# Optimization experiments

Hardware: AMD Instinct MI355X
Metric: run time of the kernel (lower is better)

## Reference

```python
import jax, jax.numpy as jnp
import numpy as np

B, T, D = 2, 2048, 1024
H, HKV, HD = 16, 4, 64
N_REP = H // HKV
SKIP_WINDOW, GLOBAL_TOKENS = 24, 8
NEG_INF = -1.0e9
ROPE_BASE = 10000.0


def rope_tables(seq_len, head_dim):
    # timm build_rotary_pos_embed (in_pixels=False, 1 spatial dim): dim//4 freq bands,
    # repeat_interleave(2) -> head_dim//2, then cat twice -> head_dim.
    nb = head_dim // 4
    inv_freq = 1.0 / (ROPE_BASE ** (jnp.arange(nb, dtype=jnp.float32) / nb))
    ang = jnp.arange(seq_len, dtype=jnp.float32)[:, None] * inv_freq[None, :]  # [T, nb]
    sin_h = jnp.repeat(jnp.sin(ang), 2, axis=-1)  # [T, HD/2]
    cos_h = jnp.repeat(jnp.cos(ang), 2, axis=-1)
    sin = jnp.concatenate([sin_h, sin_h], axis=-1)  # [T, HD]
    cos = jnp.concatenate([cos_h, cos_h], axis=-1)
    return cos, sin


def rotate_half(x):
    x1, x2 = jnp.split(x, 2, axis=-1)
    return jnp.concatenate([-x2, x1], axis=-1)


def apply_rope(x, cos, sin):
    # x: [B, H, T, HD]; cos/sin: [T, HD]
    return x * cos[None, None] + rotate_half(x) * sin[None, None]


def skip_mask(seq_len):
    half_window = SKIP_WINDOW // 2
    i = jnp.arange(seq_len)[:, None]
    j = jnp.arange(seq_len)[None, :]
    allowed = (jnp.abs(i - j) <= half_window) | (i < GLOBAL_TOKENS) | (j < GLOBAL_TOKENS)
    return jnp.where(allowed, 0.0, NEG_INF).astype(jnp.float32)  # [T, T]


def setup_inputs() -> dict:
    key = jax.random.key(0)
    ks = jax.random.split(key, 10)
    s = 0.02
    return {
        "x": jax.random.normal(ks[0], (B, T, D), jnp.float32),
        "Wq": jax.random.normal(ks[1], (D, D), jnp.float32) * s,
        "bq": jax.random.normal(ks[2], (D,), jnp.float32) * s,
        "Wk": jax.random.normal(ks[3], (D, HKV * HD), jnp.float32) * s,
        "bk": jax.random.normal(ks[4], (HKV * HD,), jnp.float32) * s,
        "Wv": jax.random.normal(ks[5], (D, HKV * HD), jnp.float32) * s,
        "bv": jax.random.normal(ks[6], (HKV * HD,), jnp.float32) * s,
        "Wo": jax.random.normal(ks[7], (D, D), jnp.float32) * s,
        "bo": jax.random.normal(ks[8], (D,), jnp.float32) * s,
        "head_weights": 1.0 + jax.random.normal(ks[9], (H,), jnp.float32) * 0.1,
    }


def reference(x, Wq, bq, Wk, bk, Wv, bv, Wo, bo, head_weights):
    Bx, Tx, _ = x.shape
    q = (x @ Wq + bq).reshape(Bx, Tx, H, HD).transpose(0, 2, 1, 3)       # [B,H,T,HD]
    k = (x @ Wk + bk).reshape(Bx, Tx, HKV, HD).transpose(0, 2, 1, 3)     # [B,HKV,T,HD]
    v = (x @ Wv + bv).reshape(Bx, Tx, HKV, HD).transpose(0, 2, 1, 3)

    cos, sin = rope_tables(Tx, HD)
    q = apply_rope(q, cos, sin)
    k = apply_rope(k, cos, sin)

    # GQA: repeat kv heads (each kv head gets n_rep consecutive q-head copies)
    k = jnp.repeat(k, N_REP, axis=1)  # [B,H,T,HD]
    v = jnp.repeat(v, N_REP, axis=1)

    # per-head learned q scaling
    q = q * head_weights[None, :, None, None]

    mask = skip_mask(Tx)  # [T,T], additive
    scale = 1.0 / jnp.sqrt(jnp.float32(HD))
    scores = jnp.einsum("bhqd,bhkd->bhqk", q, k) * scale + mask[None, None]
    attn = jax.nn.softmax(scores, axis=-1)
    out = jnp.einsum("bhqk,bhkd->bhqd", attn, v)          # [B,H,T,HD]
    out = out.transpose(0, 2, 1, 3).reshape(Bx, Tx, D)    # [B,T,D]
    return out @ Wo + bo
```

## Files before the change

### kernel.cpp

```cpp
#include <hip/hip_runtime.h>
#include <hip/hip_bf16.h>
#include <math.h>

typedef short bf16x8 __attribute__((ext_vector_type(8)));
typedef float f32x4 __attribute__((ext_vector_type(4)));
typedef unsigned short u16;
typedef u16 u16x4 __attribute__((ext_vector_type(4)));
typedef u16 u16x8 __attribute__((ext_vector_type(8)));

#define DEV static __device__ __forceinline__
#define GLB __attribute__((address_space(1)))
#define LDS __attribute__((address_space(3)))

#if defined(__has_builtin)
#if __has_builtin(__builtin_amdgcn_fdot2_f32_bf16)
#define HAS_BF16_DOT2 1
#endif
#endif

#ifdef HAS_BF16_DOT2
typedef __bf16 bf16x2 __attribute__((ext_vector_type(2)));
#endif

DEV float bf2f(u16 u) { union { unsigned int i; float f; } v; v.i = ((unsigned int)u) << 16; return v.f; }
DEV u16 f2bf(float f) {
  union { float fl; unsigned int i; } v; v.fl = f;
  return (u16)((v.i + 0x7FFFu + ((v.i >> 16) & 1u)) >> 16);
}

DEV float dot8(u16x8 k, u16x8 q, float acc) {
#ifdef HAS_BF16_DOT2
  union { u16x8 u; bf16x2 b[4]; } ku, qu;
  ku.u = k; qu.u = q;
#pragma unroll
  for (int e = 0; e < 4; ++e)
    acc = __builtin_amdgcn_fdot2_f32_bf16(ku.b[e], qu.b[e], acc, false);
#else
#pragma unroll
  for (int e = 0; e < 8; ++e) acc = fmaf(bf2f(k[e]), bf2f(q[e]), acc);
#endif
  return acc;
}

__global__ __launch_bounds__(256) void prepw_kernel(
    const float* __restrict__ x, const float* __restrict__ bq,
    const float* __restrict__ bk, const float* __restrict__ bv,
    float* __restrict__ biascat, float* __restrict__ cosT, float* __restrict__ sinT,
    u16* __restrict__ xbf,
    const float* __restrict__ wq, const float* __restrict__ wk,
    const float* __restrict__ wv, const float* __restrict__ wo,
    u16* __restrict__ wcat, u16* __restrict__ wot)
{
  __shared__ float tile[32][33];
  if (blockIdx.x < 4358) {
    int idx = blockIdx.x * 256 + threadIdx.x;
    const int NX = (4096 * 1024) / 4;
    if (idx < NX) {
      const float4 v = ((const float4*)x)[idx];
      u16x4 o;
      o[0] = f2bf(v.x); o[1] = f2bf(v.y); o[2] = f2bf(v.z); o[3] = f2bf(v.w);
      *((u16x4*)xbf + idx) = o;
    } else if (idx < NX + 1536) {
      int n = idx - NX;
      biascat[n] = (n < 1024) ? bq[n] : (n < 1280 ? bk[n - 1024] : bv[n - 1280]);
    } else if (idx < NX + 1536 + 65536) {
      int e = idx - NX - 1536;
      int t = e >> 5, dh = e & 31;
      double invf = pow(10000.0, -(double)(dh >> 1) / 16.0);
      double ang = (double)t * invf;
      cosT[e] = (float)cos(ang);
      sinT[e] = (float)sin(ang);
    }
  } else {
    const int idx = blockIdx.x - 4358;
    const int z = idx >> 10;
    const int rem = idx & 1023;
    const int bx = rem & 31, by = rem >> 5;
    const float* src; u16* dst; int N; int roff;
    if (z == 0)      { src = wq; dst = wcat; N = 1024; roff = 0; }
    else if (z == 1) { src = wk; dst = wcat; N = 256;  roff = 1024; }
    else if (z == 2) { src = wv; dst = wcat; N = 256;  roff = 1280; }
    else             { src = wo; dst = wot;  N = 1024; roff = 0; }
    const int n0 = bx << 5;
    if (n0 >= N) return;
    const int k0 = by << 5;
    const int tx = threadIdx.x & 31, ty = threadIdx.x >> 5;
#pragma unroll
    for (int r = 0; r < 32; r += 8)
      tile[ty + r][tx] = src[(size_t)(k0 + ty + r) * N + n0 + tx];
    __syncthreads();
#pragma unroll
    for (int r = 0; r < 32; r += 8)
      dst[((size_t)(roff + n0 + ty + r) << 10) + k0 + tx] = f2bf(tile[tx][ty + r]);
  }
}

__global__ __launch_bounds__(256) void gemm_kernel(
    const u16* __restrict__ A, const u16* __restrict__ Bt, int K, int mode,
    const float* __restrict__ bias_cat, u16* __restrict__ qbuf, u16* __restrict__ kbufT,
    u16* __restrict__ vbufT, const float* __restrict__ bo, float* __restrict__ outp,
    const float* __restrict__ cosT, const float* __restrict__ sinT,
    const float* __restrict__ hw)
{
  __shared__ alignas(16) char ldsA[16384];
  __shared__ alignas(16) char ldsB[8192];
  const int tid = threadIdx.x;
  const int lane = tid & 63, wid = tid >> 6;
  const int l15 = lane & 15, lg = lane >> 4;
  const int wm = wid << 5;
  const size_t K_ = (size_t)K;
  const u16* Apan = A + (size_t)blockIdx.y * 128 * K_;
  const u16* Bpan = Bt + (size_t)blockIdx.x * 64 * K_;

  f32x4 acc[2][4];
  const f32x4 fz = {0.f, 0.f, 0.f, 0.f};
#pragma unroll
  for (int mt = 0; mt < 2; ++mt)
#pragma unroll
    for (int nt = 0; nt < 4; ++nt) acc[mt][nt] = fz;

  for (int k0 = 0; k0 < K; k0 += 64) {
#pragma unroll
    for (int i = 0; i < 4; ++i) {
      const int grp = i * 4 + wid;
      const int c = grp * 64 + lane;
      const int r = c >> 3, k8 = (c & 7) << 3;
      const u16* ga = Apan + (size_t)r * K_ + k0 + k8;
      __builtin_amdgcn_global_load_lds((const GLB void*)ga, (LDS void*)(ldsA + grp * 1024), 16, 0, 0);
      if (i < 2) {
        const u16* gb = Bpan + (size_t)r * K_ + k0 + k8;
        __builtin_amdgcn_global_load_lds((const GLB void*)gb, (LDS void*)(ldsB + grp * 1024), 16, 0, 0);
      }
    }
    __syncthreads();
#pragma unroll
    for (int ks = 0; ks < 2; ++ks) {
      const int kbyte = ks * 64 + lg * 16;
      bf16x8 af[2], bfr[4];
#pragma unroll
      for (int mt = 0; mt < 2; ++mt)
        af[mt] = *(const bf16x8*)(ldsA + (wm + mt * 16 + l15) * 128 + kbyte);
#pragma unroll
      for (int nt = 0; nt < 4; ++nt)
        bfr[nt] = *(const bf16x8*)(ldsB + (nt * 16 + l15) * 128 + kbyte);
#pragma unroll
      for (int mt = 0; mt < 2; ++mt)
#pragma unroll
        for (int nt = 0; nt < 4; ++nt)
          acc[mt][nt] = __builtin_amdgcn_mfma_f32_16x16x32_bf16(af[mt], bfr[nt], acc[mt][nt], 0, 0, 0);
    }
    __syncthreads();
  }

  const int rb = blockIdx.y * 128 + wm + (lg << 2);
  const int bx = blockIdx.x;

  if (mode == 0) {
    const bool isQ = (bx < 16);
    const bool isV = (bx >= 20);
    const float hws = isQ ? hw[bx] * 0.125f : 1.0f;
    float bia[4];
#pragma unroll
    for (int nt = 0; nt < 4; ++nt) bia[nt] = bias_cat[bx * 64 + l15 + nt * 16];
    if (isV) {
#pragma unroll
      for (int mt = 0; mt < 2; ++mt) {
        const int r0 = rb + mt * 16;
        const int bb = r0 >> 11, t0 = r0 & 2047;
        const size_t base = ((size_t)(bb * 4 + (bx - 20))) << 17;
#pragma unroll
        for (int nt = 0; nt < 4; ++nt) {
          u16x4 pk;
#pragma unroll
          for (int j = 0; j < 4; ++j) pk[j] = f2bf(acc[mt][nt][j] + bia[nt]);
          const int d = l15 + nt * 16;
          *(u16x4*)(vbufT + base + (size_t)d * 2048 + t0) = pk;
        }
      }
    } else {
#pragma unroll
      for (int mt = 0; mt < 2; ++mt) {
#pragma unroll
        for (int j = 0; j < 4; ++j) {
          const int r = rb + mt * 16 + j;
          const int bb = r >> 11, t = r & 2047;
          float z[4];
#pragma unroll
          for (int nt = 0; nt < 4; ++nt) z[nt] = acc[mt][nt][j] + bia[nt];
          const float c0 = cosT[(t << 5) + l15],      s0 = sinT[(t << 5) + l15];
          const float c1 = cosT[(t << 5) + l15 + 16], s1 = sinT[(t << 5) + l15 + 16];
          const float n0 = (z[0] * c0 - z[2] * s0) * hws;
          const float n2 = (z[2] * c0 + z[0] * s0) * hws;
          const float n1 = (z[1] * c1 - z[3] * s1) * hws;
          const float n3 = (z[3] * c1 + z[1] * s1) * hws;
          z[0] = n0; z[1] = n1; z[2] = n2; z[3] = n3;
#pragma unroll
          for (int nt = 0; nt < 4; ++nt) {
            const int d = l15 + nt * 16;
            const u16 val = f2bf(z[nt]);
            if (isQ) {
              qbuf[(((size_t)(bb * 16 + bx) * 2048 + t) << 6) + d] = val;
            } else {
              kbufT[(((size_t)(bb * 4 + (bx - 16))) << 17) + ((d >> 3) << 14) + (t << 3) + (d & 7)] = val;
            }
          }
        }
      }
    }
  } else {
#pragma unroll
    for (int nt = 0; nt < 4; ++nt) {
      const int c = bx * 64 + l15 + nt * 16;
      const float bias = bo[c];
#pragma unroll
      for (int mt = 0; mt < 2; ++mt) {
#pragma unroll
        for (int j = 0; j < 4; ++j) {
          const int r = rb + mt * 16 + j;
          outp[(size_t)r * 1024 + c] = acc[mt][nt][j] + bias;
        }
      }
    }
  }
}

__global__ __launch_bounds__(256) void attn_band_kernel(
    const u16* __restrict__ qbuf, const u16* __restrict__ kbufT,
    const u16* __restrict__ vbufT, u16* __restrict__ obuf)
{
  __shared__ alignas(16) u16 plds[4][16][64];
  const int tid = threadIdx.x;
  const int lane = tid & 63, w = tid >> 6;
  const int l15 = lane & 15, lg = lane >> 4;
  const f32x4 fz = {0.f, 0.f, 0.f, 0.f};
  u16* pw = (u16*)plds[w];

  const int gw = blockIdx.x * 4 + w;
  const int k = gw & 127;
  const int h = (gw >> 7) & 15;
  const int b = gw >> 11;
  const int i0 = 8 + k * 16;
  const int a = i0 - 16;
  const int hkv = h >> 2;

  const u16* KpT = kbufT + (((size_t)(b * 4 + hkv)) << 17);
  const u16* VpT = vbufT + (((size_t)(b * 4 + hkv)) << 17);
  const u16* Qp  = qbuf + (((size_t)(b * 16 + h)) << 17);

  bf16x8 qa[2];
#pragma unroll
  for (int ch = 0; ch < 2; ++ch)
    qa[ch] = *(const bf16x8*)(Qp + (size_t)(i0 + l15) * 64 + ch * 32 + lg * 8);

  int slotj[4];
#pragma unroll
  for (int mt = 0; mt < 4; ++mt) {
    const int t = mt * 16 + l15;
    int j = (t < 8) ? t : a + t - 8;
    slotj[mt] = j < 0 ? 0 : (j > 2047 ? 2047 : j);
  }

  f32x4 s[4];
#pragma unroll
  for (int mt = 0; mt < 4; ++mt) s[mt] = fz;
#pragma unroll
  for (int ch = 0; ch < 2; ++ch) {
#pragma unroll
    for (int mt = 0; mt < 4; ++mt) {
      bf16x8 kf = *(const bf16x8*)(KpT + ((size_t)(ch * 4 + lg) << 14) + (slotj[mt] << 3));
      s[mt] = __builtin_amdgcn_mfma_f32_16x16x32_bf16(qa[ch], kf, s[mt], 0, 0, 0);
    }
  }

#pragma unroll
  for (int mt = 0; mt < 4; ++mt) {
    const int t = mt * 16 + l15;
    const int j = (t < 8) ? t : a + t - 8;
#pragma unroll
    for (int jr = 0; jr < 4; ++jr) {
      const int i = i0 + lg * 4 + jr;
      bool ok;
      if (t < 8) ok = true;
      else ok = (j >= 8) && (j < 2048) && (j >= i - 12) && (j <= i + 12);
      if (!ok) s[mt][jr] = -1e30f;
    }
  }
  float pinvl[4];
#pragma unroll
  for (int jr = 0; jr < 4; ++jr) {
    float m = fmaxf(fmaxf(s[0][jr], s[1][jr]), fmaxf(s[2][jr], s[3][jr]));
#pragma unroll
    for (int sh = 1; sh <= 8; sh <<= 1) m = fmaxf(m, __shfl_xor(m, sh));
    float sum = 0.f;
#pragma unroll
    for (int mt = 0; mt < 4; ++mt) {
      const float p = __expf(s[mt][jr] - m);
      s[mt][jr] = p;
      sum += p;
    }
#pragma unroll
    for (int sh = 1; sh <= 8; sh <<= 1) sum += __shfl_xor(sum, sh);
    pinvl[jr] = 1.f / sum;
  }

#pragma unroll
  for (int mt = 0; mt < 4; ++mt) {
    const int t = mt * 16 + l15;
#pragma unroll
    for (int jr = 0; jr < 4; ++jr) {
      const int q = lg * 4 + jr;
      pw[q * 64 + (t ^ ((q & 7) << 3))] = f2bf(s[mt][jr] * pinvl[jr]);
    }
  }

  bf16x8 paf[2];
#pragma unroll
  for (int ch = 0; ch < 2; ++ch)
    paf[ch] = *(const bf16x8*)(pw + l15 * 64 + ((ch * 32 + lg * 8) ^ ((l15 & 7) << 3)));

  f32x4 oacc[4];
#pragma unroll
  for (int db = 0; db < 4; ++db) oacc[db] = fz;
  __builtin_amdgcn_s_setprio(1);
#pragma unroll
  for (int db = 0; db < 4; ++db) {
#pragma unroll
    for (int ch = 0; ch < 2; ++ch) {
      const int sl0 = ch * 32 + lg * 8;
      int j0 = (sl0 < 8) ? 0 : a + sl0 - 8;
      j0 = j0 < 0 ? 0 : (j0 > 2040 ? 2040 : j0);
      bf16x8 vf = *(const bf16x8*)(VpT + (size_t)(db * 16 + l15) * 2048 + j0);
      oacc[db] = __builtin_amdgcn_mfma_f32_16x16x32_bf16(paf[ch], vf, oacc[db], 0, 0, 0);
    }
  }
  __builtin_amdgcn_s_setprio(0);

#pragma unroll
  for (int jr = 0; jr < 4; ++jr) {
    const int i = i0 + lg * 4 + jr;
    if (i < 2048) {
      const size_t rowo = ((size_t)(b * 2048 + i)) << 10;
#pragma unroll
      for (int db = 0; db < 4; ++db)
        obuf[rowo + h * 64 + db * 16 + l15] = f2bf(oacc[db][jr]);
    }
  }
}

__global__ __launch_bounds__(64) void attn_globp_kernel(
    const u16* __restrict__ qbuf, const u16* __restrict__ kbufT,
    const u16* __restrict__ vbufT,
    float* __restrict__ pm, float* __restrict__ pl, float* __restrict__ po)
{
  __shared__ alignas(16) u16 plds[16][64];
  const int kc = blockIdx.x;
  const int hkv = blockIdx.y & 3;
  const int i = blockIdx.y >> 2;
  const int b = blockIdx.z;
  const int lane = threadIdx.x;
  const u16* KpT = kbufT + (((size_t)(b * 4 + hkv)) << 17);
  const u16* VpT = vbufT + (((size_t)(b * 4 + hkv)) << 17);
  const u16* Qr0 = qbuf + ((((size_t)(b * 16 + hkv * 4 + 0)) * 2048 + i) << 6);
  const u16* Qr1 = qbuf + ((((size_t)(b * 16 + hkv * 4 + 1)) * 2048 + i) << 6);
  const u16* Qr2 = qbuf + ((((size_t)(b * 16 + hkv * 4 + 2)) * 2048 + i) << 6);
  const u16* Qr3 = qbuf + ((((size_t)(b * 16 + hkv * 4 + 3)) * 2048 + i) << 6);

  const int j = (kc << 6) + lane;
  float s0 = 0.f, s1 = 0.f, s2 = 0.f, s3 = 0.f;
#pragma unroll
  for (int d8 = 0; d8 < 8; ++d8) {
    u16x8 k8 = *(const u16x8*)(KpT + (d8 << 14) + (j << 3));
    u16x8 q0 = *(const u16x8*)(Qr0 + d8 * 8);
    u16x8 q1 = *(const u16x8*)(Qr1 + d8 * 8);
    u16x8 q2 = *(const u16x8*)(Qr2 + d8 * 8);
    u16x8 q3 = *(const u16x8*)(Qr3 + d8 * 8);
    s0 = dot8(k8, q0, s0);
    s1 = dot8(k8, q1, s1);
    s2 = dot8(k8, q2, s2);
    s3 = dot8(k8, q3, s3);
  }
  float m0 = s0, m1 = s1, m2 = s2, m3 = s3;
#pragma unroll
  for (int sh = 32; sh >= 1; sh >>= 1) {
    m0 = fmaxf(m0, __shfl_xor(m0, sh));
    m1 = fmaxf(m1, __shfl_xor(m1, sh));
    m2 = fmaxf(m2, __shfl_xor(m2, sh));
    m3 = fmaxf(m3, __shfl_xor(m3, sh));
  }
  float p0 = __expf(s0 - m0), p1 = __expf(s1 - m1), p2 = __expf(s2 - m2), p3 = __expf(s3 - m3);
  float l0 = p0, l1 = p1, l2 = p2, l3 = p3;
#pragma unroll
  for (int sh = 32; sh >= 1; sh >>= 1) {
    l0 += __shfl_xor(l0, sh);
    l1 += __shfl_xor(l1, sh);
    l2 += __shfl_xor(l2, sh);
    l3 += __shfl_xor(l3, sh);
  }

  u16* pw = (u16*)plds;
  pw[0 * 64 + (lane ^ 0)]  = f2bf(p0);
  pw[1 * 64 + (lane ^ 8)]  = f2bf(p1);
  pw[2 * 64 + (lane ^ 16)] = f2bf(p2);
  pw[3 * 64 + (lane ^ 24)] = f2bf(p3);

  const int l15 = lane & 15, lg = lane >> 4;
  bf16x8 paf[2];
#pragma unroll
  for (int ch = 0; ch < 2; ++ch)
    paf[ch] = *(const bf16x8*)(pw + l15 * 64 + ((ch * 32 + lg * 8) ^ ((l15 & 7) << 3)));

  f32x4 oacc[4];
  const f32x4 fz = {0.f, 0.f, 0.f, 0.f};
#pragma unroll
  for (int db = 0; db < 4; ++db) oacc[db] = fz;
#pragma unroll
  for (int db = 0; db < 4; ++db) {
#pragma unroll
    for (int ch = 0; ch < 2; ++ch) {
      const int j0 = (kc << 6) + ch * 32 + lg * 8;
      bf16x8 vf = *(const bf16x8*)(VpT + (size_t)(db * 16 + l15) * 2048 + j0);
      oacc[db] = __builtin_amdgcn_mfma_f32_16x16x32_bf16(paf[ch], vf, oacc[db], 0, 0, 0);
    }
  }

  const int part = (((b * 4 + hkv) * 8 + i) << 5) + kc;
  if (lane == 0) {
    pm[part * 4 + 0] = m0; pm[part * 4 + 1] = m1; pm[part * 4 + 2] = m2; pm[part * 4 + 3] = m3;
    pl[part * 4 + 0] = l0; pl[part * 4 + 1] = l1; pl[part * 4 + 2] = l2; pl[part * 4 + 3] = l3;
  }
  if (lg == 0) {
    float* pob = po + (((size_t)part << 2) << 6);
#pragma unroll
    for (int db = 0; db < 4; ++db)
#pragma unroll
      for (int h = 0; h < 4; ++h)
        pob[h * 64 + db * 16 + l15] = oacc[db][h];
  }
}

__global__ __launch_bounds__(256) void attn_globm_kernel(
    const float* __restrict__ pm, const float* __restrict__ pl,
    const float* __restrict__ po, u16* __restrict__ obuf)
{
  const int idx = blockIdx.x;
  const int i = idx & 7;
  const int hkv = (idx >> 3) & 3;
  const int b = idx >> 5;
  const int tid = threadIdx.x;
  const int lane = tid & 63, h = tid >> 6;
  const int base = ((b * 4 + hkv) * 8 + i) << 5;

  float M = -1e30f;
#pragma unroll 8
  for (int kc = 0; kc < 32; ++kc) M = fmaxf(M, pm[(base + kc) * 4 + h]);
  float L = 0.f, O = 0.f;
#pragma unroll 8
  for (int kc = 0; kc < 32; ++kc) {
    float sc = __expf(pm[(base + kc) * 4 + h] - M);
    L += pl[(base + kc) * 4 + h] * sc;
    O = fmaf(po[((((size_t)(base + kc) << 2) + h) << 6) + lane], sc, O);
  }
  obuf[(((size_t)(b * 2048 + i)) << 10) + (hkv * 4 + h) * 64 + lane] = f2bf(O / L);
}

extern "C" void kernel_launch(void* const* d_in, const int* in_sizes, int n_in,
                              void* d_out, int out_size, void* d_ws, size_t ws_size,
                              hipStream_t stream) {
  const float* x  = (const float*)d_in[0];
  const float* Wq = (const float*)d_in[1];
  const float* bq = (const float*)d_in[2];
  const float* Wk = (const float*)d_in[3];
  const float* bk = (const float*)d_in[4];
  const float* Wv = (const float*)d_in[5];
  const float* bv = (const float*)d_in[6];
  const float* Wo = (const float*)d_in[7];
  const float* bo = (const float*)d_in[8];
  const float* hw = (const float*)d_in[9];
  float* out = (float*)d_out;

  char* ws = (char*)d_ws;
  size_t off = 0;
  auto alloc = [&](size_t bytes) { char* p = ws + off; off += (bytes + 255) & ~(size_t)255; return p; };
  u16* xbf    = (u16*)alloc((size_t)4096 * 1024 * 2);
  u16* wcat   = (u16*)alloc((size_t)1536 * 1024 * 2);
  u16* wot    = (u16*)alloc((size_t)1024 * 1024 * 2);
  float* biascat = (float*)alloc(1536 * 4);
  float* cosT = (float*)alloc(65536 * 4);
  float* sinT = (float*)alloc(65536 * 4);
  u16* qbuf   = (u16*)alloc((size_t)2 * 16 * 2048 * 64 * 2);
  u16* kbufT  = (u16*)alloc((size_t)2 * 4 * 2048 * 64 * 2);
  u16* vbufT  = (u16*)alloc((size_t)2 * 4 * 2048 * 64 * 2);
  float* pm   = (float*)alloc((size_t)2048 * 4 * 4);
  float* pl   = (float*)alloc((size_t)2048 * 4 * 4);
  float* po   = (float*)alloc((size_t)2048 * 4 * 64 * 4);
  u16* obuf   = xbf;

  prepw_kernel<<<8454, 256, 0, stream>>>(x, bq, bk, bv, biascat, cosT, sinT, xbf,
                                         Wq, Wk, Wv, Wo, wcat, wot);
  gemm_kernel<<<dim3(24, 32), 256, 0, stream>>>(xbf, wcat, 1024, 0, biascat, qbuf, kbufT, vbufT,
                                                nullptr, nullptr, cosT, sinT, hw);
  attn_band_kernel<<<1024, 256, 0, stream>>>(qbuf, kbufT, vbufT, obuf);
  attn_globp_kernel<<<dim3(32, 32, 2), 64, 0, stream>>>(qbuf, kbufT, vbufT, pm, pl, po);
  attn_globm_kernel<<<64, 256, 0, stream>>>(pm, pl, po, obuf);
  gemm_kernel<<<dim3(16, 32), 256, 0, stream>>>(obuf, wot, 1024, 1, nullptr, nullptr, nullptr,
                                               nullptr, bo, out, nullptr, nullptr, nullptr);
}
```

Before: 86.93 us.

## Merge band and global-partial attention kernels; XCD-swizzle GEMM block mapping

The band-attention and global-partial attention kernels are merged into one launch. The first 1024 blocks run the band path and the remaining blocks each run four 64-thread global-partial waves, which removes one kernel launch and lets the two paths overlap on the GPU. The GEMM grid is flattened to 1D with a remap of block index modulo 8, which appears to group tiles per XCD and improve L2 reuse of the A and B panels. The risks are heterogeneous blocks within one grid and the changed tile order affecting cache behaviour.

```diff
diff --git a/kernel.cpp b/kernel.cpp
--- a/kernel.cpp
+++ b/kernel.cpp
@@ -109,8 +109,15 @@
   const int l15 = lane & 15, lg = lane >> 4;
   const int wm = wid << 5;
   const size_t K_ = (size_t)K;
-  const u16* Apan = A + (size_t)blockIdx.y * 128 * K_;
-  const u16* Bpan = Bt + (size_t)blockIdx.x * 64 * K_;
+
+  const int nbx = (mode == 0) ? 24 : 16;
+  const int cpx = gridDim.x >> 3;
+  const int swz = (blockIdx.x & 7) * cpx + (blockIdx.x >> 3);
+  const int bx = swz % nbx;
+  const int by = swz / nbx;
+
+  const u16* Apan = A + (size_t)by * 128 * K_;
+  const u16* Bpan = Bt + (size_t)bx * 64 * K_;
 
   f32x4 acc[2][4];
   const f32x4 fz = {0.f, 0.f, 0.f, 0.f};
@@ -152,8 +159,7 @@
     __syncthreads();
   }
 
-  const int rb = blockIdx.y * 128 + wm + (lg << 2);
-  const int bx = blockIdx.x;
+  const int rb = by * 128 + wm + (lg << 2);
 
   if (mode == 0) {
     const bool isQ = (bx < 16);
@@ -224,9 +230,10 @@
   }
 }
 
-__global__ __launch_bounds__(256) void attn_band_kernel(
+__global__ __launch_bounds__(256) void attn_comb_kernel(
     const u16* __restrict__ qbuf, const u16* __restrict__ kbufT,
-    const u16* __restrict__ vbufT, u16* __restrict__ obuf)
+    const u16* __restrict__ vbufT, u16* __restrict__ obuf,
+    float* __restrict__ pm, float* __restrict__ pl, float* __restrict__ po)
 {
   __shared__ alignas(16) u16 plds[4][16][64];
   const int tid = threadIdx.x;
@@ -235,206 +242,199 @@
   const f32x4 fz = {0.f, 0.f, 0.f, 0.f};
   u16* pw = (u16*)plds[w];
 
-  const int gw = blockIdx.x * 4 + w;
-  const int k = gw & 127;
-  const int h = (gw >> 7) & 15;
-  const int b = gw >> 11;
-  const int i0 = 8 + k * 16;
-  const int a = i0 - 16;
-  const int hkv = h >> 2;
-
-  const u16* KpT = kbufT + (((size_t)(b * 4 + hkv)) << 17);
-  const u16* VpT = vbufT + (((size_t)(b * 4 + hkv)) << 17);
-  const u16* Qp  = qbuf + (((size_t)(b * 16 + h)) << 17);
-
-  bf16x8 qa[2];
-#pragma unroll
-  for (int ch = 0; ch < 2; ++ch)
-    qa[ch] = *(const bf16x8*)(Qp + (size_t)(i0 + l15) * 64 + ch * 32 + lg * 8);
-
-  int slotj[4];
-#pragma unroll
-  for (int mt = 0; mt < 4; ++mt) {
-    const int t = mt * 16 + l15;
-    int j = (t < 8) ? t : a + t - 8;
-    slotj[mt] = j < 0 ? 0 : (j > 2047 ? 2047 : j);
-  }
-
-  f32x4 s[4];
-#pragma unroll
-  for (int mt = 0; mt < 4; ++mt) s[mt] = fz;
-#pragma unroll
-  for (int ch = 0; ch < 2; ++ch) {
+  if (blockIdx.x < 1024) {
+    const int gw = blockIdx.x * 4 + w;
+    const int k = gw & 127;
+    const int h = (gw >> 7) & 15;
+    const int b = gw >> 11;
+    const int i0 = 8 + k * 16;
+    const int a = i0 - 16;
+    const int hkv = h >> 2;
+
+    const u16* KpT = kbufT + (((size_t)(b * 4 + hkv)) << 17);
+    const u16* VpT = vbufT + (((size_t)(b * 4 + hkv)) << 17);
+    const u16* Qp  = qbuf + (((size_t)(b * 16 + h)) << 17);
+
+    bf16x8 qa[2];
+#pragma unroll
+    for (int ch = 0; ch < 2; ++ch)
+      qa[ch] = *(const bf16x8*)(Qp + (size_t)(i0 + l15) * 64 + ch * 32 + lg * 8);
+
+    int slotj[4];
 #pragma unroll
     for (int mt = 0; mt < 4; ++mt) {
-      bf16x8 kf = *(const bf16x8*)(KpT + ((size_t)(ch * 4 + lg) << 14) + (slotj[mt] << 3));
-      s[mt] = __builtin_amdgcn_mfma_f32_16x16x32_bf16(qa[ch], kf, s[mt], 0, 0, 0);
-    }
-  }
-
-#pragma unroll
-  for (int mt = 0; mt < 4; ++mt) {
-    const int t = mt * 16 + l15;
-    const int j = (t < 8) ? t : a + t - 8;
+      const int t = mt * 16 + l15;
+      int j = (t < 8) ? t : a + t - 8;
+      slotj[mt] = j < 0 ? 0 : (j > 2047 ? 2047 : j);
+    }
+
+    f32x4 s[4];
+#pragma unroll
+    for (int mt = 0; mt < 4; ++mt) s[mt] = fz;
+#pragma unroll
+    for (int ch = 0; ch < 2; ++ch) {
+#pragma unroll
+      for (int mt = 0; mt < 4; ++mt) {
+        bf16x8 kf = *(const bf16x8*)(KpT + ((size_t)(ch * 4 + lg) << 14) + (slotj[mt] << 3));
+        s[mt] = __builtin_amdgcn_mfma_f32_16x16x32_bf16(qa[ch], kf, s[mt], 0, 0, 0);
+      }
+    }
+
+#pragma unroll
+    for (int mt = 0; mt < 4; ++mt) {
+      const int t = mt * 16 + l15;
+      const int j = (t < 8) ? t : a + t - 8;
+#pragma unroll
+      for (int jr = 0; jr < 4; ++jr) {
+        const int i = i0 + lg * 4 + jr;
+        bool ok;
+        if (t < 8) ok = true;
+        else ok = (j >= 8) && (j < 2048) && (j >= i - 12) && (j <= i + 12);
+        if (!ok) s[mt][jr] = -1e30f;
+      }
+    }
+    float pinvl[4];
+#pragma unroll
+    for (int jr = 0; jr < 4; ++jr) {
+      float m = fmaxf(fmaxf(s[0][jr], s[1][jr]), fmaxf(s[2][jr], s[3][jr]));
+#pragma unroll
+      for (int sh = 1; sh <= 8; sh <<= 1) m = fmaxf(m, __shfl_xor(m, sh));
+      float sum = 0.f;
+#pragma unroll
+      for (int mt = 0; mt < 4; ++mt) {
+        const float p = __expf(s[mt][jr] - m);
+        s[mt][jr] = p;
+        sum += p;
+      }
+#pragma unroll
+      for (int sh = 1; sh <= 8; sh <<= 1) sum += __shfl_xor(sum, sh);
+      pinvl[jr] = 1.f / sum;
+    }
+
+#pragma unroll
+    for (int mt = 0; mt < 4; ++mt) {
+      const int t = mt * 16 + l15;
+#pragma unroll
+      for (int jr = 0; jr < 4; ++jr) {
+        const int q = lg * 4 + jr;
+        pw[q * 64 + (t ^ ((q & 7) << 3))] = f2bf(s[mt][jr] * pinvl[jr]);
+      }
+    }
+
+    bf16x8 paf[2];
+#pragma unroll
+    for (int ch = 0; ch < 2; ++ch)
+      paf[ch] = *(const bf16x8*)(pw + l15 * 64 + ((ch * 32 + lg * 8) ^ ((l15 & 7) << 3)));
+
+    f32x4 oacc[4];
+#pragma unroll
+    for (int db = 0; db < 4; ++db) oacc[db] = fz;
+    __builtin_amdgcn_s_setprio(1);
+#pragma unroll
+    for (int db = 0; db < 4; ++db) {
+#pragma unroll
+      for (int ch = 0; ch < 2; ++ch) {
+        const int sl0 = ch * 32 + lg * 8;
+        int j0 = (sl0 < 8) ? 0 : a + sl0 - 8;
+        j0 = j0 < 0 ? 0 : (j0 > 2040 ? 2040 : j0);
+        bf16x8 vf = *(const bf16x8*)(VpT + (size_t)(db * 16 + l15) * 2048 + j0);
+        oacc[db] = __builtin_amdgcn_mfma_f32_16x16x32_bf16(paf[ch], vf, oacc[db], 0, 0, 0);
+      }
+    }
+    __builtin_amdgcn_s_setprio(0);
+
 #pragma unroll
     for (int jr = 0; jr < 4; ++jr) {
       const int i = i0 + lg * 4 + jr;
-      bool ok;
-      if (t < 8) ok = true;
-      else ok = (j >= 8) && (j < 2048) && (j >= i - 12) && (j <= i + 12);
-      if (!ok) s[mt][jr] = -1e30f;
-    }
-  }
-  float pinvl[4];
-#pragma unroll
-  for (int jr = 0; jr < 4; ++jr) {
-    float m = fmaxf(fmaxf(s[0][jr], s[1][jr]), fmaxf(s[2][jr], s[3][jr]));
-#pragma unroll
-    for (int sh = 1; sh <= 8; sh <<= 1) m = fmaxf(m, __shfl_xor(m, sh));
-    float sum = 0.f;
-#pragma unroll
-    for (int mt = 0; mt < 4; ++mt) {
-      const float p = __expf(s[mt][jr] - m);
-      s[mt][jr] = p;
-      sum += p;
-    }
-#pragma unroll
-    for (int sh = 1; sh <= 8; sh <<= 1) sum += __shfl_xor(sum, sh);
-    pinvl[jr] = 1.f / sum;
-  }
-
-#pragma unroll
-  for (int mt = 0; mt < 4; ++mt) {
-    const int t = mt * 16 + l15;
-#pragma unroll
-    for (int jr = 0; jr < 4; ++jr) {
-      const int q = lg * 4 + jr;
-      pw[q * 64 + (t ^ ((q & 7) << 3))] = f2bf(s[mt][jr] * pinvl[jr]);
-    }
-  }
-
-  bf16x8 paf[2];
-#pragma unroll
-  for (int ch = 0; ch < 2; ++ch)
-    paf[ch] = *(const bf16x8*)(pw + l15 * 64 + ((ch * 32 + lg * 8) ^ ((l15 & 7) << 3)));
-
-  f32x4 oacc[4];
-#pragma unroll
-  for (int db = 0; db < 4; ++db) oacc[db] = fz;
-  __builtin_amdgcn_s_setprio(1);
-#pragma unroll
-  for (int db = 0; db < 4; ++db) {
-#pragma unroll
-    for (int ch = 0; ch < 2; ++ch) {
-      const int sl0 = ch * 32 + lg * 8;
-      int j0 = (sl0 < 8) ? 0 : a + sl0 - 8;
-      j0 = j0 < 0 ? 0 : (j0 > 2040 ? 2040 : j0);
-      bf16x8 vf = *(const bf16x8*)(VpT + (size_t)(db * 16 + l15) * 2048 + j0);
-      oacc[db] = __builtin_amdgcn_mfma_f32_16x16x32_bf16(paf[ch], vf, oacc[db], 0, 0, 0);
-    }
-  }
-  __builtin_amdgcn_s_setprio(0);
-
-#pragma unroll
-  for (int jr = 0; jr < 4; ++jr) {
-    const int i = i0 + lg * 4 + jr;
-    if (i < 2048) {
-      const size_t rowo = ((size_t)(b * 2048 + i)) << 10;
+      if (i < 2048) {
+        const size_t rowo = ((size_t)(b * 2048 + i)) << 10;
+#pragma unroll
+        for (int db = 0; db < 4; ++db)
+          obuf[rowo + h * 64 + db * 16 + l15] = f2bf(oacc[db][jr]);
+      }
+    }
+  } else {
+    const int u = (blockIdx.x - 1024) * 4 + w;
+    const int kc = u & 31;
+    const int yi = (u >> 5) & 31;
+    const int b = u >> 10;
+    const int hkv = yi & 3;
+    const int i = yi >> 2;
+    const u16* KpT = kbufT + (((size_t)(b * 4 + hkv)) << 17);
+    const u16* VpT = vbufT + (((size_t)(b * 4 + hkv)) << 17);
+    const u16* Qr0 = qbuf + ((((size_t)(b * 16 + hkv * 4 + 0)) * 2048 + i) << 6);
+    const u16* Qr1 = qbuf + ((((size_t)(b * 16 + hkv * 4 + 1)) * 2048 + i) << 6);
+    const u16* Qr2 = qbuf + ((((size_t)(b * 16 + hkv * 4 + 2)) * 2048 + i) << 6);
+    const u16* Qr3 = qbuf + ((((size_t)(b * 16 + hkv * 4 + 3)) * 2048 + i) << 6);
+
+    const int j = (kc << 6) + lane;
+    float s0 = 0.f, s1 = 0.f, s2 = 0.f, s3 = 0.f;
+#pragma unroll
+    for (int d8 = 0; d8 < 8; ++d8) {
+      u16x8 k8 = *(const u16x8*)(KpT + (d8 << 14) + (j << 3));
+      u16x8 q0 = *(const u16x8*)(Qr0 + d8 * 8);
+      u16x8 q1 = *(const u16x8*)(Qr1 + d8 * 8);
+      u16x8 q2 = *(const u16x8*)(Qr2 + d8 * 8);
+      u16x8 q3 = *(const u16x8*)(Qr3 + d8 * 8);
+      s0 = dot8(k8, q0, s0);
+      s1 = dot8(k8, q1, s1);
+      s2 = dot8(k8, q2, s2);
+      s3 = dot8(k8, q3, s3);
+    }
+    float m0 = s0, m1 = s1, m2 = s2, m3 = s3;
+#pragma unroll
+    for (int sh = 32; sh >= 1; sh >>= 1) {
+      m0 = fmaxf(m0, __shfl_xor(m0, sh));
+      m1 = fmaxf(m1, __shfl_xor(m1, sh));
+      m2 = fmaxf(m2, __shfl_xor(m2, sh));
+      m3 = fmaxf(m3, __shfl_xor(m3, sh));
+    }
+    float p0 = __expf(s0 - m0), p1 = __expf(s1 - m1), p2 = __expf(s2 - m2), p3 = __expf(s3 - m3);
+    float l0 = p0, l1 = p1, l2 = p2, l3 = p3;
+#pragma unroll
+    for (int sh = 32; sh >= 1; sh >>= 1) {
+      l0 += __shfl_xor(l0, sh);
+      l1 += __shfl_xor(l1, sh);
+      l2 += __shfl_xor(l2, sh);
+      l3 += __shfl_xor(l3, sh);
+    }
+
+    pw[0 * 64 + (lane ^ 0)]  = f2bf(p0);
+    pw[1 * 64 + (lane ^ 8)]  = f2bf(p1);
+    pw[2 * 64 + (lane ^ 16)] = f2bf(p2);
+    pw[3 * 64 + (lane ^ 24)] = f2bf(p3);
+
+    bf16x8 paf[2];
+#pragma unroll
+    for (int ch = 0; ch < 2; ++ch)
+      paf[ch] = *(const bf16x8*)(pw + l15 * 64 + ((ch * 32 + lg * 8) ^ ((l15 & 7) << 3)));
+
+    f32x4 oacc[4];
+#pragma unroll
+    for (int db = 0; db < 4; ++db) oacc[db] = fz;
+#pragma unroll
+    for (int db = 0; db < 4; ++db) {
+#pragma unroll
+      for (int ch = 0; ch < 2; ++ch) {
+        const int j0 = (kc << 6) + ch * 32 + lg * 8;
+        bf16x8 vf = *(const bf16x8*)(VpT + (size_t)(db * 16 + l15) * 2048 + j0);
+        oacc[db] = __builtin_amdgcn_mfma_f32_16x16x32_bf16(paf[ch], vf, oacc[db], 0, 0, 0);
+      }
+    }
+
+    const int part = (((b * 4 + hkv) * 8 + i) << 5) + kc;
+    if (lane == 0) {
+      pm[part * 4 + 0] = m0; pm[part * 4 + 1] = m1; pm[part * 4 + 2] = m2; pm[part * 4 + 3] = m3;
+      pl[part * 4 + 0] = l0; pl[part * 4 + 1] = l1; pl[part * 4 + 2] = l2; pl[part * 4 + 3] = l3;
+    }
+    if (lg == 0) {
+      float* pob = po + (((size_t)part << 2) << 6);
 #pragma unroll
       for (int db = 0; db < 4; ++db)
-        obuf[rowo + h * 64 + db * 16 + l15] = f2bf(oacc[db][jr]);
-    }
-  }
-}
-
-__global__ __launch_bounds__(64) void attn_globp_kernel(
-    const u16* __restrict__ qbuf, const u16* __restrict__ kbufT,
-    const u16* __restrict__ vbufT,
-    float* __restrict__ pm, float* __restrict__ pl, float* __restrict__ po)
-{
-  __shared__ alignas(16) u16 plds[16][64];
-  const int kc = blockIdx.x;
-  const int hkv = blockIdx.y & 3;
-  const int i = blockIdx.y >> 2;
-  const int b = blockIdx.z;
-  const int lane = threadIdx.x;
-  const u16* KpT = kbufT + (((size_t)(b * 4 + hkv)) << 17);
-  const u16* VpT = vbufT + (((size_t)(b * 4 + hkv)) << 17);
-  const u16* Qr0 = qbuf + ((((size_t)(b * 16 + hkv * 4 + 0)) * 2048 + i) << 6);
-  const u16* Qr1 = qbuf + ((((size_t)(b * 16 + hkv * 4 + 1)) * 2048 + i) << 6);
-  const u16* Qr2 = qbuf + ((((size_t)(b * 16 + hkv * 4 + 2)) * 2048 + i) << 6);
-  const u16* Qr3 = qbuf + ((((size_t)(b * 16 + hkv * 4 + 3)) * 2048 + i) << 6);
-
-  const int j = (kc << 6) + lane;
-  float s0 = 0.f, s1 = 0.f, s2 = 0.f, s3 = 0.f;
-#pragma unroll
-  for (int d8 = 0; d8 < 8; ++d8) {
-    u16x8 k8 = *(const u16x8*)(KpT + (d8 << 14) + (j << 3));
-    u16x8 q0 = *(const u16x8*)(Qr0 + d8 * 8);
-    u16x8 q1 = *(const u16x8*)(Qr1 + d8 * 8);
-    u16x8 q2 = *(const u16x8*)(Qr2 + d8 * 8);
-    u16x8 q3 = *(const u16x8*)(Qr3 + d8 * 8);
-    s0 = dot8(k8, q0, s0);
-    s1 = dot8(k8, q1, s1);
-    s2 = dot8(k8, q2, s2);
-    s3 = dot8(k8, q3, s3);
-  }
-  float m0 = s0, m1 = s1, m2 = s2, m3 = s3;
-#pragma unroll
-  for (int sh = 32; sh >= 1; sh >>= 1) {
-    m0 = fmaxf(m0, __shfl_xor(m0, sh));
-    m1 = fmaxf(m1, __shfl_xor(m1, sh));
-    m2 = fmaxf(m2, __shfl_xor(m2, sh));
-    m3 = fmaxf(m3, __shfl_xor(m3, sh));
-  }
-  float p0 = __expf(s0 - m0), p1 = __expf(s1 - m1), p2 = __expf(s2 - m2), p3 = __expf(s3 - m3);
-  float l0 = p0, l1 = p1, l2 = p2, l3 = p3;
-#pragma unroll
-  for (int sh = 32; sh >= 1; sh >>= 1) {
-    l0 += __shfl_xor(l0, sh);
-    l1 += __shfl_xor(l1, sh);
-    l2 += __shfl_xor(l2, sh);
-    l3 += __shfl_xor(l3, sh);
-  }
-
-  u16* pw = (u16*)plds;
-  pw[0 * 64 + (lane ^ 0)]  = f2bf(p0);
-  pw[1 * 64 + (lane ^ 8)]  = f2bf(p1);
-  pw[2 * 64 + (lane ^ 16)] = f2bf(p2);
-  pw[3 * 64 + (lane ^ 24)] = f2bf(p3);
-
-  const int l15 = lane & 15, lg = lane >> 4;
-  bf16x8 paf[2];
-#pragma unroll
-  for (int ch = 0; ch < 2; ++ch)
-    paf[ch] = *(const bf16x8*)(pw + l15 * 64 + ((ch * 32 + lg * 8) ^ ((l15 & 7) << 3)));
-
-  f32x4 oacc[4];
-  const f32x4 fz = {0.f, 0.f, 0.f, 0.f};
-#pragma unroll
-  for (int db = 0; db < 4; ++db) oacc[db] = fz;
-#pragma unroll
-  for (int db = 0; db < 4; ++db) {
-#pragma unroll
-    for (int ch = 0; ch < 2; ++ch) {
-      const int j0 = (kc << 6) + ch * 32 + lg * 8;
-      bf16x8 vf = *(const bf16x8*)(VpT + (size_t)(db * 16 + l15) * 2048 + j0);
-      oacc[db] = __builtin_amdgcn_mfma_f32_16x16x32_bf16(paf[ch], vf, oacc[db], 0, 0, 0);
-    }
-  }
-
-  const int part = (((b * 4 + hkv) * 8 + i) << 5) + kc;
-  if (lane == 0) {
-    pm[part * 4 + 0] = m0; pm[part * 4 + 1] = m1; pm[part * 4 + 2] = m2; pm[part * 4 + 3] = m3;
-    pl[part * 4 + 0] = l0; pl[part * 4 + 1] = l1; pl[part * 4 + 2] = l2; pl[part * 4 + 3] = l3;
-  }
-  if (lg == 0) {
-    float* pob = po + (((size_t)part << 2) << 6);
-#pragma unroll
-    for (int db = 0; db < 4; ++db)
-#pragma unroll
-      for (int h = 0; h < 4; ++h)
-        pob[h * 64 + db * 16 + l15] = oacc[db][h];
+#pragma unroll
+        for (int h = 0; h < 4; ++h)
+          pob[h * 64 + db * 16 + l15] = oacc[db][h];
+    }
   }
 }
 
@@ -497,11 +497,10 @@
 
   prepw_kernel<<<8454, 256, 0, stream>>>(x, bq, bk, bv, biascat, cosT, sinT, xbf,
                                          Wq, Wk, Wv, Wo, wcat, wot);
-  gemm_kernel<<<dim3(24, 32), 256, 0, stream>>>(xbf, wcat, 1024, 0, biascat, qbuf, kbufT, vbufT,
-                                                nullptr, nullptr, cosT, sinT, hw);
-  attn_band_kernel<<<1024, 256, 0, stream>>>(qbuf, kbufT, vbufT, obuf);
-  attn_globp_kernel<<<dim3(32, 32, 2), 64, 0, stream>>>(qbuf, kbufT, vbufT, pm, pl, po);
+  gemm_kernel<<<768, 256, 0, stream>>>(xbf, wcat, 1024, 0, biascat, qbuf, kbufT, vbufT,
+                                       nullptr, nullptr, cosT, sinT, hw);
+  attn_comb_kernel<<<1536, 256, 0, stream>>>(qbuf, kbufT, vbufT, obuf, pm, pl, po);
   attn_globm_kernel<<<64, 256, 0, stream>>>(pm, pl, po, obuf);
-  gemm_kernel<<<dim3(16, 32), 256, 0, stream>>>(obuf, wot, 1024, 1, nullptr, nullptr, nullptr,
-                                               nullptr, bo, out, nullptr, nullptr, nullptr);
-}
+  gemm_kernel<<<512, 256, 0, stream>>>(obuf, wot, 1024, 1, nullptr, nullptr, nullptr,
+                                       nullptr, bo, out, nullptr, nullptr, nullptr);
+}
```

Result: no change. 85.32 us (-1.9%).
